# Kernel tuning notes

Hardware: AMD Instinct MI355X
Metric: run time of the kernel (lower is better)

Reference implementation:

```python
import jax, jax.numpy as jnp
import numpy as np

N_NODES = 50000
N_GRAPHS = 64
IN_DIM, HIDDEN, OUT_DIM = 2063, 256, 128
E_L, E_G = 800000, 1600000


def setup_inputs() -> dict:
    key = jax.random.key(0)
    ks = jax.random.split(key, 16)
    x = jax.random.normal(ks[0], (N_NODES, IN_DIM), dtype=jnp.float32)
    edge_index_l = jax.random.randint(ks[1], (2, E_L), 0, N_NODES, dtype=jnp.int64)
    edge_index_g = jax.random.randint(ks[2], (2, E_G), 0, N_NODES, dtype=jnp.int64)
    batch = jnp.sort(jax.random.randint(ks[3], (N_NODES,), 0, N_GRAPHS, dtype=jnp.int64))

    def glorot(k, shape):
        scale = jnp.sqrt(2.0 / (shape[0] + shape[1])).astype(jnp.float32)
        return jax.random.normal(k, shape, dtype=jnp.float32) * scale

    return {
        "x": x,
        "edge_index_l": edge_index_l,
        "edge_index_g": edge_index_g,
        "batch": batch,
        "W_l1": glorot(ks[4], (IN_DIM, HIDDEN)), "b_l1": jnp.zeros((HIDDEN,), jnp.float32),
        "W_l2": glorot(ks[5], (HIDDEN, OUT_DIM)), "b_l2": jnp.zeros((OUT_DIM,), jnp.float32),
        "W_g1": glorot(ks[6], (IN_DIM, HIDDEN)), "b_g1": jnp.zeros((HIDDEN,), jnp.float32),
        "W_g2": glorot(ks[7], (HIDDEN, OUT_DIM)), "b_g2": jnp.zeros((OUT_DIM,), jnp.float32),
        "W_fuse": glorot(ks[8], (2 * OUT_DIM, OUT_DIM)), "b_fuse": jnp.zeros((OUT_DIM,), jnp.float32),
    }


def gcn_conv(x, edge_index, W, b):
    # PyG GCNConv: add self loops, symmetric D^{-1/2}(A+I)D^{-1/2} normalization,
    # linear transform then scatter-add aggregation at target nodes.
    n = x.shape[0]
    loops = jnp.arange(n, dtype=edge_index.dtype)
    src = jnp.concatenate([edge_index[0], loops])
    dst = jnp.concatenate([edge_index[1], loops])
    deg = jax.ops.segment_sum(jnp.ones_like(dst, dtype=x.dtype), dst, num_segments=n)
    dinv = jax.lax.rsqrt(deg)  # deg >= 1 due to self loops
    norm = dinv[src] * dinv[dst]  # [E+n]
    h = x @ W  # [n, out]
    msg = h[src] * norm[:, None]  # gather + scale
    return jax.ops.segment_sum(msg, dst, num_segments=n) + b


def global_mean_pool(x, batch, num_graphs):
    sums = jax.ops.segment_sum(x, batch, num_segments=num_graphs)
    cnt = jax.ops.segment_sum(jnp.ones((x.shape[0],), x.dtype), batch, num_segments=num_graphs)
    return sums / jnp.maximum(cnt, 1.0)[:, None]


def reference(x, edge_index_l, edge_index_g, batch,
              W_l1, b_l1, W_l2, b_l2, W_g1, b_g1, W_g2, b_g2, W_fuse, b_fuse):
    # dropout is identity in eval mode
    xl = jax.nn.relu(gcn_conv(x, edge_index_l, W_l1, b_l1))
    xl = gcn_conv(xl, edge_index_l, W_l2, b_l2)
    xl = global_mean_pool(xl, batch, N_GRAPHS)

    xg = jax.nn.relu(gcn_conv(x, edge_index_g, W_g1, b_g1))
    xg = gcn_conv(xg, edge_index_g, W_g2, b_g2)
    xg = global_mean_pool(xg, batch, N_GRAPHS)

    out = jnp.concatenate([xl, xg], axis=1)  # [G, 2*out_dim]
    return jax.nn.relu(out @ W_fuse + b_fuse)
```

## Files before the change

kernel.cpp:

```cpp
#include <hip/hip_runtime.h>
#include <hip/hip_bf16.h>
#include <cstdint>
#include <cstddef>


#define N_NODES 50000
#define N_GRAPHS 64
#define IN_DIM 2063
#define HIDDEN 256
#define OUT_DIM 128
#define EDGES_L 800000
#define EDGES_G 1600000
#define HCOLS 512
#define KPAD 2112
#define MPAD 50048
#define PCH 256
#define NCHUNK ((N_NODES + PCH - 1) / PCH)

#define QUARTER 12544
#define SL_L 64
#define SL_G 128
#define EPS 12500
#define HBLOCKS (4 * (SL_L + SL_G))

typedef __attribute__((ext_vector_type(8))) __bf16 bf16x8;
typedef __attribute__((ext_vector_type(4))) float f32x4;

__device__ __forceinline__ float bf2f(unsigned short u) {
  union { unsigned int i; float f; } c; c.i = ((unsigned int)u) << 16; return c.f;
}
__device__ __forceinline__ unsigned short f2bf(float f) {
  __hip_bfloat16 h = __float2bfloat16(f);
  return *reinterpret_cast<unsigned short*>(&h);
}

__global__ void k_cvt_x(const float* __restrict__ x, unsigned short* __restrict__ xb) {
  const int G = KPAD / 4;
  long long i = (long long)blockIdx.x * blockDim.x + threadIdx.x;
  if (i >= (long long)MPAD * G) return;
  int row = (int)(i / G);
  int k = (int)(i - (long long)row * G) * 4;
  ushort4 o;
  float v0 = 0.f, v1 = 0.f, v2 = 0.f, v3 = 0.f;
  if (row < N_NODES) {
    const float* xr = x + (size_t)row * IN_DIM;
    if (k + 0 < IN_DIM) v0 = xr[k + 0];
    if (k + 1 < IN_DIM) v1 = xr[k + 1];
    if (k + 2 < IN_DIM) v2 = xr[k + 2];
    if (k + 3 < IN_DIM) v3 = xr[k + 3];
  }
  o.x = f2bf(v0); o.y = f2bf(v1); o.z = f2bf(v2); o.w = f2bf(v3);
  *(ushort4*)(xb + (size_t)row * KPAD + k) = o;
}

__global__ void k_cvt_w(const float* __restrict__ Wl, const float* __restrict__ Wg,
                        unsigned short* __restrict__ Wt) {
  int i = blockIdx.x * blockDim.x + threadIdx.x;
  if (i >= HCOLS * KPAD) return;
  int n = i / KPAD;
  int k = i - n * KPAD;
  float v = 0.f;
  if (k < IN_DIM) {
    v = (n < HIDDEN) ? Wl[(size_t)k * HIDDEN + n] : Wg[(size_t)k * HIDDEN + (n - HIDDEN)];
  }
  Wt[(size_t)n * KPAD + k] = f2bf(v);
}

__launch_bounds__(256)
__global__ void k_hist(const int* __restrict__ dstL, const int* __restrict__ dstG,
                       int* __restrict__ partL, int* __restrict__ partG) {
  __shared__ int hist[QUARTER];
  const int i = blockIdx.x;
  const int* __restrict__ dst;
  int slice, q;
  int* __restrict__ part;
  if (i < 4 * SL_L) {
    slice = i >> 2; q = i & 3;
    dst = dstL;
    part = partL + (size_t)(slice * 4 + q) * QUARTER;
  } else {
    int j = i - 4 * SL_L;
    slice = j >> 2; q = j & 3;
    dst = dstG;
    part = partG + (size_t)(slice * 4 + q) * QUARTER;
  }
  for (int t = threadIdx.x; t < QUARTER; t += 256) hist[t] = 0;
  __syncthreads();
  const int e0 = slice * EPS;
  const int qbase = q * QUARTER;
  for (int e = e0 + threadIdx.x; e < e0 + EPS; e += 256) {
    int d = dst[e] - qbase;
    if ((unsigned)d < QUARTER) atomicAdd(&hist[d], 1);
  }
  __syncthreads();
  for (int t = threadIdx.x; t < QUARTER; t += 256) part[t] = hist[t];
}

__global__ void k_prefix(int* __restrict__ partL, int* __restrict__ partG,
                         const int* __restrict__ batch, int* __restrict__ degL,
                         int* __restrict__ degG, float* __restrict__ dinvL,
                         float* __restrict__ dinvG, float* __restrict__ cL,
                         float* __restrict__ cG) {
  int t = blockIdx.x * blockDim.x + threadIdx.x;
  if (t >= 8 * QUARTER) return;
  const int b = t / (4 * QUARTER);
  const int n = t - b * 4 * QUARTER;
  const int q = n / QUARTER, loc = n - q * QUARTER;
  const int NS = b ? SL_G : SL_L;
  int* p = (b ? partG : partL) + (size_t)q * QUARTER + loc;
  int run = 0;
  for (int s = 0; s < NS; s++) {
    int* pp = p + (size_t)s * 4 * QUARTER;
    int v = *pp;
    *pp = run;
    run += v;
  }
  if (n < N_NODES) {
    float d = 1.0f / sqrtf((float)(run + 1));
    if (b == 0) {
      degL[n] = run; dinvL[n] = d; cL[(size_t)n * 64 + batch[n]] = d * d;
    } else {
      degG[n] = run; dinvG[n] = d; cG[(size_t)n * 64 + batch[n]] = d * d;
    }
  }
}

__global__ void k_bounds(const int* __restrict__ batch, int* __restrict__ start) {
  int n = blockIdx.x * blockDim.x + threadIdx.x;
  if (n >= N_NODES) return;
  int bn = batch[n];
  int bp = n ? batch[n - 1] : -1;
  for (int g = bp + 1; g <= bn; g++) start[g] = n;
  if (n == N_NODES - 1)
    for (int g = bn + 1; g <= N_GRAPHS; g++) start[g] = N_NODES;
}

__global__ void k_scan1(const int* __restrict__ degL, const int* __restrict__ degG,
                        int* __restrict__ rowL, int* __restrict__ rowG) {
  __shared__ int part[1024];
  const int t = threadIdx.x;
  const int* __restrict__ deg = blockIdx.x ? degG : degL;
  int* __restrict__ row = blockIdx.x ? rowG : rowL;
  const int c0 = t * 49;
  int s = 0;
  for (int j = 0; j < 49; j++) {
    int idx = c0 + j;
    s += (idx < N_NODES) ? deg[idx] : 0;
  }
  part[t] = s;
  __syncthreads();
  for (int ofs = 1; ofs < 1024; ofs <<= 1) {
    int v = (t >= ofs) ? part[t - ofs] : 0;
    __syncthreads();
    part[t] += v;
    __syncthreads();
  }
  int run = (t > 0) ? part[t - 1] : 0;
  for (int j = 0; j < 49; j++) {
    int idx = c0 + j;
    if (idx < N_NODES) { row[idx] = run; run += deg[idx]; }
  }
  if (t == 1023) row[N_NODES] = part[1023];
}

__launch_bounds__(256)
__global__ void k_scatter2(const int* __restrict__ srcL, const int* __restrict__ dstL,
                           const int* __restrict__ srcG, const int* __restrict__ dstG,
                           const int* __restrict__ partL, const int* __restrict__ partG,
                           const int* __restrict__ rowL, const int* __restrict__ rowG,
                           const float* __restrict__ dinvL, const float* __restrict__ dinvG,
                           const int* __restrict__ batch, int2* __restrict__ erL,
                           int2* __restrict__ erG, float* __restrict__ cL,
                           float* __restrict__ cG) {
  __shared__ int hist[QUARTER];
  const int i = blockIdx.x;
  const int *src, *dst, *part, *row;
  const float* dinv;
  int2* er;
  float* c;
  int slice, q;
  if (i < 4 * SL_L) {
    slice = i >> 2; q = i & 3;
    src = srcL; dst = dstL; row = rowL; dinv = dinvL; er = erL; c = cL;
    part = partL + (size_t)(slice * 4 + q) * QUARTER;
  } else {
    int j = i - 4 * SL_L;
    slice = j >> 2; q = j & 3;
    src = srcG; dst = dstG; row = rowG; dinv = dinvG; er = erG; c = cG;
    part = partG + (size_t)(slice * 4 + q) * QUARTER;
  }
  for (int t = threadIdx.x; t < QUARTER; t += 256) hist[t] = 0;
  __syncthreads();
  const int e0 = slice * EPS;
  const int qbase = q * QUARTER;
  for (int e = e0 + threadIdx.x; e < e0 + EPS; e += 256) {
    int d = dst[e];
    int loc = d - qbase;
    if ((unsigned)loc < QUARTER) {
      int s = src[e];
      int rank = atomicAdd(&hist[loc], 1);
      int pos = row[d] + part[loc] + rank;
      float nrm = dinv[s] * dinv[d];
      er[pos] = make_int2(s, __float_as_int(nrm));
      atomicAdd(&c[(size_t)s * 64 + batch[d]], nrm);
    }
  }
}

__launch_bounds__(256)
__global__ void k_mfma_gemm(const unsigned short* __restrict__ Xb,
                            const unsigned short* __restrict__ Wt,
                            unsigned short* __restrict__ H) {
  __shared__ __align__(16) char lds[32768];
  const int tid = threadIdx.x;
  const int lane = tid & 63;
  const int wave = tid >> 6;
  const int wr = wave >> 1, wc = wave & 1;
  const int brow = blockIdx.y * 128;
  const int bcol = blockIdx.x * 128;

  f32x4 acc[4][4];
  const f32x4 zero = {0.f, 0.f, 0.f, 0.f};
#pragma unroll
  for (int m = 0; m < 4; m++)
#pragma unroll
    for (int n = 0; n < 4; n++) acc[m][n] = zero;

  int rowA[4], kcS[4], ldsOff[4];
#pragma unroll
  for (int i = 0; i < 4; i++) {
    int s = (i * 4 + wave) * 64 + lane;
    int row = s >> 3;
    int c = s & 7;
    rowA[i] = row;
    kcS[i] = (c ^ (row & 7)) * 8;
    ldsOff[i] = ((i * 4 + wave) * 64) * 16;
  }

  const int fr = lane & 15;
  const int fq = lane >> 4;
  const int arow0 = wr * 64 + fr;
  const int brow0 = wc * 64 + fr;
  const int sw = lane & 7;

  for (int t = 0; t < KPAD / 64; ++t) {
    const int k0 = t * 64;
#pragma unroll
    for (int i = 0; i < 4; i++) {
      const unsigned short* g = Xb + (size_t)(brow + rowA[i]) * KPAD + k0 + kcS[i];
      __builtin_amdgcn_global_load_lds(
          (const __attribute__((address_space(1))) void*)g,
          (__attribute__((address_space(3))) void*)(lds + ldsOff[i]), 16, 0, 0);
    }
#pragma unroll
    for (int i = 0; i < 4; i++) {
      const unsigned short* g = Wt + (size_t)(bcol + rowA[i]) * KPAD + k0 + kcS[i];
      __builtin_amdgcn_global_load_lds(
          (const __attribute__((address_space(1))) void*)g,
          (__attribute__((address_space(3))) void*)(lds + 16384 + ldsOff[i]), 16, 0, 0);
    }
    __syncthreads();

#pragma unroll
    for (int kk = 0; kk < 2; kk++) {
      const int cidx = ((kk * 4 + fq) ^ sw) * 16;
      bf16x8 av[4], bv[4];
#pragma unroll
      for (int m = 0; m < 4; m++)
        av[m] = *(const bf16x8*)(lds + (arow0 + m * 16) * 128 + cidx);
#pragma unroll
      for (int n = 0; n < 4; n++)
        bv[n] = *(const bf16x8*)(lds + 16384 + (brow0 + n * 16) * 128 + cidx);
#pragma unroll
      for (int m = 0; m < 4; m++)
#pragma unroll
        for (int n = 0; n < 4; n++)
          acc[m][n] = __builtin_amdgcn_mfma_f32_16x16x32_bf16(av[m], bv[n], acc[m][n], 0, 0, 0);
    }
    __syncthreads();
  }

#pragma unroll
  for (int m = 0; m < 4; m++) {
    const int r0 = brow + wr * 64 + m * 16 + fq * 4;
#pragma unroll
    for (int n = 0; n < 4; n++) {
      const int col = bcol + wc * 64 + n * 16 + fr;
#pragma unroll
      for (int j = 0; j < 4; j++) {
        int r = r0 + j;
        if (r < N_NODES) H[(size_t)r * HCOLS + col] = f2bf(acc[m][n][j]);
      }
    }
  }
}

__global__ void k_agg(const unsigned short* __restrict__ h,
                      const float* __restrict__ dinvL, const float* __restrict__ dinvG,
                      const int* __restrict__ rowL, const int* __restrict__ rowG,
                      const int2* __restrict__ erL, const int2* __restrict__ erG,
                      const float* __restrict__ biasL, const float* __restrict__ biasG,
                      unsigned short* __restrict__ xl) {
  const int br = blockIdx.y;
  const int node = blockIdx.x * 4 + (threadIdx.x >> 6);
  const int lane = threadIdx.x & 63;
  const float* __restrict__ dinv = br ? dinvG : dinvL;
  const int* __restrict__ rp = br ? rowG : rowL;
  const int2* __restrict__ er = br ? erG : erL;
  const float* __restrict__ bias = br ? biasG : biasL;
  const int off = br ? 256 : 0;
  const size_t lcol = off + lane * 4;

  float di = dinv[node];
  float w0 = di * di;
  ushort4 u = *(const ushort4*)(h + (size_t)node * HCOLS + lcol);
  float a0 = w0 * bf2f(u.x), a1 = w0 * bf2f(u.y), a2 = w0 * bf2f(u.z), a3 = w0 * bf2f(u.w);

  int e = rp[node];
  const int e1 = rp[node + 1];
  for (; e + 8 <= e1; e += 8) {
    int2 r[8];
    ushort4 v[8];
#pragma unroll
    for (int j = 0; j < 8; j++) r[j] = er[e + j];
#pragma unroll
    for (int j = 0; j < 8; j++)
      v[j] = *(const ushort4*)(h + (size_t)r[j].x * HCOLS + lcol);
#pragma unroll
    for (int j = 0; j < 8; j++) {
      float w = __int_as_float(r[j].y);
      a0 = fmaf(w, bf2f(v[j].x), a0);
      a1 = fmaf(w, bf2f(v[j].y), a1);
      a2 = fmaf(w, bf2f(v[j].z), a2);
      a3 = fmaf(w, bf2f(v[j].w), a3);
    }
  }
  for (; e + 4 <= e1; e += 4) {
    int2 r[4];
    ushort4 v[4];
#pragma unroll
    for (int j = 0; j < 4; j++) r[j] = er[e + j];
#pragma unroll
    for (int j = 0; j < 4; j++)
      v[j] = *(const ushort4*)(h + (size_t)r[j].x * HCOLS + lcol);
#pragma unroll
    for (int j = 0; j < 4; j++) {
      float w = __int_as_float(r[j].y);
      a0 = fmaf(w, bf2f(v[j].x), a0);
      a1 = fmaf(w, bf2f(v[j].y), a1);
      a2 = fmaf(w, bf2f(v[j].z), a2);
      a3 = fmaf(w, bf2f(v[j].w), a3);
    }
  }
  for (; e < e1; e++) {
    int2 r = er[e];
    float w = __int_as_float(r.y);
    ushort4 v = *(const ushort4*)(h + (size_t)r.x * HCOLS + lcol);
    a0 = fmaf(w, bf2f(v.x), a0);
    a1 = fmaf(w, bf2f(v.y), a1);
    a2 = fmaf(w, bf2f(v.z), a2);
    a3 = fmaf(w, bf2f(v.w), a3);
  }
  float4 b = *(const float4*)(bias + lane * 4);
  ushort4 o;
  o.x = f2bf(fmaxf(a0 + b.x, 0.f));
  o.y = f2bf(fmaxf(a1 + b.y, 0.f));
  o.z = f2bf(fmaxf(a2 + b.z, 0.f));
  o.w = f2bf(fmaxf(a3 + b.w, 0.f));
  *(ushort4*)(xl + (size_t)node * HCOLS + lcol) = o;
}

__launch_bounds__(256)
__global__ void k_pool2(const unsigned short* __restrict__ xl,
                        const float* __restrict__ cL, const float* __restrict__ cG,
                        float* __restrict__ Spart) {
  __shared__ float cs[64][64];
  const int t = threadIdx.x;
  const int chunk = blockIdx.x;
  const int br = blockIdx.y;
  const float* __restrict__ C = br ? cG : cL;
  const int xoff = br ? 256 : 0;
  const int n0 = chunk * PCH;
  float acc[64];
#pragma unroll
  for (int g = 0; g < 64; g++) acc[g] = 0.f;

  for (int tile = 0; tile < PCH; tile += 64) {
    const int base = n0 + tile;
    __syncthreads();
#pragma unroll
    for (int i = 0; i < 16; i++) {
      int idx = i * 256 + t;
      int nn = idx >> 6, gg = idx & 63;
      int node = base + nn;
      cs[nn][gg] = (node < N_NODES) ? C[(size_t)node * 64 + gg] : 0.f;
    }
    __syncthreads();
    for (int nn = 0; nn < 64; nn++) {
      int node = base + nn;
      float v = (node < N_NODES) ? bf2f(xl[(size_t)node * HCOLS + xoff + t]) : 0.f;
#pragma unroll
      for (int g4 = 0; g4 < 16; g4++) {
        float4 cv = *(const float4*)&cs[nn][g4 * 4];
        acc[g4 * 4 + 0] = fmaf(cv.x, v, acc[g4 * 4 + 0]);
        acc[g4 * 4 + 1] = fmaf(cv.y, v, acc[g4 * 4 + 1]);
        acc[g4 * 4 + 2] = fmaf(cv.z, v, acc[g4 * 4 + 2]);
        acc[g4 * 4 + 3] = fmaf(cv.w, v, acc[g4 * 4 + 3]);
      }
    }
  }
  float* sp = Spart + ((size_t)br * NCHUNK + chunk) * 16384 + t;
#pragma unroll
  for (int g = 0; g < 64; g++) sp[g * 256] = acc[g];
}

__global__ void k_pool_reduce(const float* __restrict__ Spart, float* __restrict__ S) {
  int i = blockIdx.x * blockDim.x + threadIdx.x;
  if (i >= 2 * 16384) return;
  int br = i >> 14, idx = i & 16383;
  const float* p = Spart + (size_t)br * NCHUNK * 16384 + idx;
  float s = 0.f;
  for (int ch = 0; ch < NCHUNK; ch++) s += p[(size_t)ch * 16384];
  S[i] = s;
}

__global__ void k_final(const float* __restrict__ S,
                        const float* __restrict__ Wl2, const float* __restrict__ bl2,
                        const float* __restrict__ Wg2, const float* __restrict__ bg2,
                        const float* __restrict__ Wf, const float* __restrict__ bf,
                        const int* __restrict__ start, float* __restrict__ out) {
  __shared__ float pl[OUT_DIM], pg[OUT_DIM];
  int g = blockIdx.x, t = threadIdx.x;
  float invc = 1.0f / fmaxf((float)(start[g + 1] - start[g]), 1.0f);
  const float* Sl = S + (size_t)g * HIDDEN;
  const float* Sg = S + (size_t)N_GRAPHS * HIDDEN + (size_t)g * HIDDEN;
  float al = 0.f, ag = 0.f;
  for (int k = 0; k < HIDDEN; k++) {
    al = fmaf(Sl[k], Wl2[k * OUT_DIM + t], al);
    ag = fmaf(Sg[k], Wg2[k * OUT_DIM + t], ag);
  }
  pl[t] = al * invc + bl2[t];
  pg[t] = ag * invc + bg2[t];
  __syncthreads();
  float o = bf[t];
  for (int j = 0; j < OUT_DIM; j++) {
    o = fmaf(pl[j], Wf[j * OUT_DIM + t], o);
    o = fmaf(pg[j], Wf[(OUT_DIM + j) * OUT_DIM + t], o);
  }
  out[(size_t)g * OUT_DIM + t] = fmaxf(o, 0.f);
}

extern "C" void kernel_launch(void* const* d_in, const int* in_sizes, int n_in,
                              void* d_out, int out_size, void* d_ws, size_t ws_size,
                              hipStream_t stream) {
  const float* x = (const float*)d_in[0];
  const int* el = (const int*)d_in[1];
  const int* eg = (const int*)d_in[2];
  const int* batch = (const int*)d_in[3];
  const float* Wl1 = (const float*)d_in[4];
  const float* bl1 = (const float*)d_in[5];
  const float* Wl2 = (const float*)d_in[6];
  const float* bl2 = (const float*)d_in[7];
  const float* Wg1 = (const float*)d_in[8];
  const float* bg1 = (const float*)d_in[9];
  const float* Wg2 = (const float*)d_in[10];
  const float* bg2 = (const float*)d_in[11];
  const float* Wf = (const float*)d_in[12];
  const float* bf = (const float*)d_in[13];
  float* out = (float*)d_out;
  char* ws = (char*)d_ws;

  const size_t NPAD = 200192;
  size_t off = 0;
  float* c_l = (float*)(ws + off); off += (size_t)N_NODES * 64 * 4;
  float* c_g = (float*)(ws + off); off += (size_t)N_NODES * 64 * 4;
  const size_t zero_bytes = off;
  int* start = (int*)(ws + off); off += 512;
  float* S = (float*)(ws + off); off += (size_t)2 * N_GRAPHS * HIDDEN * 4;
  int* deg_l = (int*)(ws + off); off += NPAD;
  int* deg_g = (int*)(ws + off); off += NPAD;
  float* dinv_l = (float*)(ws + off); off += NPAD;
  float* dinv_g = (float*)(ws + off); off += NPAD;
  int* row_l = (int*)(ws + off); off += NPAD;
  int* row_g = (int*)(ws + off); off += NPAD;
  int* partL = (int*)(ws + off); off += (size_t)SL_L * 4 * QUARTER * 4;
  int* partG = (int*)(ws + off); off += (size_t)SL_G * 4 * QUARTER * 4;
  int2* er_l = (int2*)(ws + off); off += (size_t)EDGES_L * 8;
  int2* er_g = (int2*)(ws + off); off += (size_t)EDGES_G * 8;
  unsigned short* xb = (unsigned short*)(ws + off); off += (size_t)MPAD * KPAD * 2;
  unsigned short* Wt = (unsigned short*)(ws + off); off += (size_t)HCOLS * KPAD * 2;
  unsigned short* h = (unsigned short*)(ws + off); off += (size_t)N_NODES * HCOLS * 2;
  unsigned short* xl = (unsigned short*)(ws + off); off += (size_t)N_NODES * HCOLS * 2;
  float* Spart = (float*)xb;

  const int* srcL = el;
  const int* dstL = el + EDGES_L;
  const int* srcG = eg;
  const int* dstG = eg + EDGES_G;

  hipMemsetAsync(ws, 0, zero_bytes, stream);

  {
    long long tot = (long long)MPAD * (KPAD / 4);
    k_cvt_x<<<(int)((tot + 255) / 256), 256, 0, stream>>>(x, xb);
    k_cvt_w<<<(HCOLS * KPAD + 255) / 256, 256, 0, stream>>>(Wl1, Wg1, Wt);
  }

  k_hist<<<HBLOCKS, 256, 0, stream>>>(dstL, dstG, partL, partG);
  k_prefix<<<(8 * QUARTER + 255) / 256, 256, 0, stream>>>(partL, partG, batch, deg_l, deg_g,
                                                          dinv_l, dinv_g, c_l, c_g);
  k_bounds<<<(N_NODES + 255) / 256, 256, 0, stream>>>(batch, start);
  k_scan1<<<2, 1024, 0, stream>>>(deg_l, deg_g, row_l, row_g);
  k_scatter2<<<HBLOCKS, 256, 0, stream>>>(srcL, dstL, srcG, dstG, partL, partG, row_l, row_g,
                                          dinv_l, dinv_g, batch, er_l, er_g, c_l, c_g);

  dim3 ggrid(4, MPAD / 128);
  k_mfma_gemm<<<ggrid, 256, 0, stream>>>(xb, Wt, h);

  dim3 agrid(N_NODES / 4, 2);
  k_agg<<<agrid, 256, 0, stream>>>(h, dinv_l, dinv_g, row_l, row_g, er_l, er_g, bl1, bg1, xl);

  dim3 pgrid(NCHUNK, 2);
  k_pool2<<<pgrid, 256, 0, stream>>>(xl, c_l, c_g, Spart);
  k_pool_reduce<<<(2 * 16384 + 255) / 256, 256, 0, stream>>>(Spart, S);

  k_final<<<N_GRAPHS, OUT_DIM, 0, stream>>>(S, Wl2, bl2, Wg2, bg2, Wf, bf, start, out);
}
```

Measured before the change: 1.036 ms.

## Fuse fp32-to-bf16 conversion of x into the GEMM and merge bounds kernel into scan

Removes the separate pass that converts x to a padded bf16 buffer. The GEMM now reads fp32 rows of x directly, converts them in registers and writes them to LDS, prefetching the next k-slice during compute. The GEMM tile becomes 64 rows by all 512 columns so each x row is read only once, with W streamed per block. The graph-bounds kernel is folded into the scan launch as extra blocks. The trade-offs are unaligned fp32 row loads, heavier W traffic per block and 72KB of LDS per block, which limits occupancy.

After: 958.8 us. 1.08x faster.

```diff
diff --git a/kernel.cpp b/kernel.cpp
--- a/kernel.cpp
+++ b/kernel.cpp
@@ -14,6 +14,7 @@
 #define HCOLS 512
 #define KPAD 2112
 #define MPAD 50048
+#define GBM 64
 #define PCH 256
 #define NCHUNK ((N_NODES + PCH - 1) / PCH)
 
@@ -32,25 +33,6 @@
 __device__ __forceinline__ unsigned short f2bf(float f) {
   __hip_bfloat16 h = __float2bfloat16(f);
   return *reinterpret_cast<unsigned short*>(&h);
-}
-
-__global__ void k_cvt_x(const float* __restrict__ x, unsigned short* __restrict__ xb) {
-  const int G = KPAD / 4;
-  long long i = (long long)blockIdx.x * blockDim.x + threadIdx.x;
-  if (i >= (long long)MPAD * G) return;
-  int row = (int)(i / G);
-  int k = (int)(i - (long long)row * G) * 4;
-  ushort4 o;
-  float v0 = 0.f, v1 = 0.f, v2 = 0.f, v3 = 0.f;
-  if (row < N_NODES) {
-    const float* xr = x + (size_t)row * IN_DIM;
-    if (k + 0 < IN_DIM) v0 = xr[k + 0];
-    if (k + 1 < IN_DIM) v1 = xr[k + 1];
-    if (k + 2 < IN_DIM) v2 = xr[k + 2];
-    if (k + 3 < IN_DIM) v3 = xr[k + 3];
-  }
-  o.x = f2bf(v0); o.y = f2bf(v1); o.z = f2bf(v2); o.w = f2bf(v3);
-  *(ushort4*)(xb + (size_t)row * KPAD + k) = o;
 }
 
 __global__ void k_cvt_w(const float* __restrict__ Wl, const float* __restrict__ Wg,
@@ -125,18 +107,19 @@
   }
 }
 
-__global__ void k_bounds(const int* __restrict__ batch, int* __restrict__ start) {
-  int n = blockIdx.x * blockDim.x + threadIdx.x;
-  if (n >= N_NODES) return;
-  int bn = batch[n];
-  int bp = n ? batch[n - 1] : -1;
-  for (int g = bp + 1; g <= bn; g++) start[g] = n;
-  if (n == N_NODES - 1)
-    for (int g = bn + 1; g <= N_GRAPHS; g++) start[g] = N_NODES;
-}
-
 __global__ void k_scan1(const int* __restrict__ degL, const int* __restrict__ degG,
-                        int* __restrict__ rowL, int* __restrict__ rowG) {
+                        int* __restrict__ rowL, int* __restrict__ rowG,
+                        const int* __restrict__ batch, int* __restrict__ start) {
+  if (blockIdx.x >= 2) {
+    int n = (blockIdx.x - 2) * 1024 + threadIdx.x;
+    if (n >= N_NODES) return;
+    int bn = batch[n];
+    int bp = n ? batch[n - 1] : -1;
+    for (int g = bp + 1; g <= bn; g++) start[g] = n;
+    if (n == N_NODES - 1)
+      for (int g = bn + 1; g <= N_GRAPHS; g++) start[g] = N_NODES;
+    return;
+  }
   __shared__ int part[1024];
   const int t = threadIdx.x;
   const int* __restrict__ deg = blockIdx.x ? degG : degL;
@@ -207,85 +190,105 @@
   }
 }
 
-__launch_bounds__(256)
-__global__ void k_mfma_gemm(const unsigned short* __restrict__ Xb,
+__launch_bounds__(256, 2)
+__global__ void k_mfma_gemm(const float* __restrict__ X,
                             const unsigned short* __restrict__ Wt,
                             unsigned short* __restrict__ H) {
-  __shared__ __align__(16) char lds[32768];
+  __shared__ __align__(16) char lds[8192 + 65536];
   const int tid = threadIdx.x;
   const int lane = tid & 63;
   const int wave = tid >> 6;
-  const int wr = wave >> 1, wc = wave & 1;
-  const int brow = blockIdx.y * 128;
-  const int bcol = blockIdx.x * 128;
-
-  f32x4 acc[4][4];
-  const f32x4 zero = {0.f, 0.f, 0.f, 0.f};
-#pragma unroll
-  for (int m = 0; m < 4; m++)
-#pragma unroll
-    for (int n = 0; n < 4; n++) acc[m][n] = zero;
-
-  int rowA[4], kcS[4], ldsOff[4];
-#pragma unroll
-  for (int i = 0; i < 4; i++) {
-    int s = (i * 4 + wave) * 64 + lane;
-    int row = s >> 3;
-    int c = s & 7;
-    rowA[i] = row;
-    kcS[i] = (c ^ (row & 7)) * 8;
-    ldsOff[i] = ((i * 4 + wave) * 64) * 16;
-  }
+  const int brow = blockIdx.x * GBM;
+
+  const int ar = tid >> 2;
+  const int ak = (tid & 3) * 16;
+  const int arow_g = brow + ar;
+  const bool aok = arow_g < N_NODES;
+  const float* __restrict__ Arow = X + (size_t)arow_g * IN_DIM;
+  const int ac0 = (tid & 3) * 2;
+  char* const awr0 = lds + ar * 128 + ((ac0 ^ (ar & 7)) * 16);
+  char* const awr1 = lds + ar * 128 + (((ac0 + 1) ^ (ar & 7)) * 16);
 
   const int fr = lane & 15;
   const int fq = lane >> 4;
-  const int arow0 = wr * 64 + fr;
-  const int brow0 = wc * 64 + fr;
-  const int sw = lane & 7;
+
+  f32x4 acc[4][8];
+  const f32x4 zero = {0.f, 0.f, 0.f, 0.f};
+#pragma unroll
+  for (int m = 0; m < 4; m++)
+#pragma unroll
+    for (int n = 0; n < 8; n++) acc[m][n] = zero;
+
+  float a[16];
+#pragma unroll
+  for (int j = 0; j < 16; j++) a[j] = aok ? Arow[ak + j] : 0.f;
 
   for (int t = 0; t < KPAD / 64; ++t) {
     const int k0 = t * 64;
 #pragma unroll
-    for (int i = 0; i < 4; i++) {
-      const unsigned short* g = Xb + (size_t)(brow + rowA[i]) * KPAD + k0 + kcS[i];
+    for (int i = 0; i < 16; i++) {
+      const int s = i * 256 + wave * 64 + lane;
+      const int row = s >> 3, cch = s & 7;
+      const unsigned short* g = Wt + (size_t)row * KPAD + k0 + ((cch ^ (row & 7)) * 8);
       __builtin_amdgcn_global_load_lds(
           (const __attribute__((address_space(1))) void*)g,
-          (__attribute__((address_space(3))) void*)(lds + ldsOff[i]), 16, 0, 0);
-    }
-#pragma unroll
-    for (int i = 0; i < 4; i++) {
-      const unsigned short* g = Wt + (size_t)(bcol + rowA[i]) * KPAD + k0 + kcS[i];
-      __builtin_amdgcn_global_load_lds(
-          (const __attribute__((address_space(1))) void*)g,
-          (__attribute__((address_space(3))) void*)(lds + 16384 + ldsOff[i]), 16, 0, 0);
+          (__attribute__((address_space(3))) void*)(lds + 8192 + (i * 256 + wave * 64) * 16),
+          16, 0, 0);
+    }
+    {
+      uint u0 = (uint)f2bf(a[0]) | ((uint)f2bf(a[1]) << 16);
+      uint u1 = (uint)f2bf(a[2]) | ((uint)f2bf(a[3]) << 16);
+      uint u2 = (uint)f2bf(a[4]) | ((uint)f2bf(a[5]) << 16);
+      uint u3 = (uint)f2bf(a[6]) | ((uint)f2bf(a[7]) << 16);
+      uint u4 = (uint)f2bf(a[8]) | ((uint)f2bf(a[9]) << 16);
+      uint u5 = (uint)f2bf(a[10]) | ((uint)f2bf(a[11]) << 16);
+      uint u6 = (uint)f2bf(a[12]) | ((uint)f2bf(a[13]) << 16);
+      uint u7 = (uint)f2bf(a[14]) | ((uint)f2bf(a[15]) << 16);
+      *(uint4*)awr0 = make_uint4(u0, u1, u2, u3);
+      *(uint4*)awr1 = make_uint4(u4, u5, u6, u7);
     }
     __syncthreads();
 
+    if (t + 1 < KPAD / 64) {
+      const int kb = k0 + 64 + ak;
+      if (aok) {
+        if (kb + 15 < IN_DIM) {
+#pragma unroll
+          for (int j = 0; j < 16; j++) a[j] = Arow[kb + j];
+        } else {
+#pragma unroll
+          for (int j = 0; j < 16; j++) a[j] = (kb + j < IN_DIM) ? Arow[kb + j] : 0.f;
+        }
+      }
+    }
+
 #pragma unroll
     for (int kk = 0; kk < 2; kk++) {
-      const int cidx = ((kk * 4 + fq) ^ sw) * 16;
-      bf16x8 av[4], bv[4];
-#pragma unroll
-      for (int m = 0; m < 4; m++)
-        av[m] = *(const bf16x8*)(lds + (arow0 + m * 16) * 128 + cidx);
-#pragma unroll
-      for (int n = 0; n < 4; n++)
-        bv[n] = *(const bf16x8*)(lds + 16384 + (brow0 + n * 16) * 128 + cidx);
-#pragma unroll
-      for (int m = 0; m < 4; m++)
-#pragma unroll
-        for (int n = 0; n < 4; n++)
-          acc[m][n] = __builtin_amdgcn_mfma_f32_16x16x32_bf16(av[m], bv[n], acc[m][n], 0, 0, 0);
+      const int kc = kk * 4 + fq;
+      bf16x8 bv[8];
+#pragma unroll
+      for (int n = 0; n < 8; n++) {
+        const int row = wave * 128 + n * 16 + fr;
+        bv[n] = *(const bf16x8*)(lds + 8192 + row * 128 + ((kc ^ (row & 7)) * 16));
+      }
+#pragma unroll
+      for (int m = 0; m < 4; m++) {
+        const int row = m * 16 + fr;
+        bf16x8 av = *(const bf16x8*)(lds + row * 128 + ((kc ^ (row & 7)) * 16));
+#pragma unroll
+        for (int n = 0; n < 8; n++)
+          acc[m][n] = __builtin_amdgcn_mfma_f32_16x16x32_bf16(av, bv[n], acc[m][n], 0, 0, 0);
+      }
     }
     __syncthreads();
   }
 
 #pragma unroll
   for (int m = 0; m < 4; m++) {
-    const int r0 = brow + wr * 64 + m * 16 + fq * 4;
-#pragma unroll
-    for (int n = 0; n < 4; n++) {
-      const int col = bcol + wc * 64 + n * 16 + fr;
+    const int r0 = brow + m * 16 + fq * 4;
+#pragma unroll
+    for (int n = 0; n < 8; n++) {
+      const int col = wave * 128 + n * 16 + fr;
 #pragma unroll
       for (int j = 0; j < 4; j++) {
         int r = r0 + j;
@@ -487,11 +490,10 @@
   int* partG = (int*)(ws + off); off += (size_t)SL_G * 4 * QUARTER * 4;
   int2* er_l = (int2*)(ws + off); off += (size_t)EDGES_L * 8;
   int2* er_g = (int2*)(ws + off); off += (size_t)EDGES_G * 8;
-  unsigned short* xb = (unsigned short*)(ws + off); off += (size_t)MPAD * KPAD * 2;
   unsigned short* Wt = (unsigned short*)(ws + off); off += (size_t)HCOLS * KPAD * 2;
   unsigned short* h = (unsigned short*)(ws + off); off += (size_t)N_NODES * HCOLS * 2;
   unsigned short* xl = (unsigned short*)(ws + off); off += (size_t)N_NODES * HCOLS * 2;
-  float* Spart = (float*)xb;
+  float* Spart = (float*)partL;
 
   const int* srcL = el;
   const int* dstL = el + EDGES_L;
@@ -500,22 +502,16 @@
 
   hipMemsetAsync(ws, 0, zero_bytes, stream);
 
-  {
-    long long tot = (long long)MPAD * (KPAD / 4);
-    k_cvt_x<<<(int)((tot + 255) / 256), 256, 0, stream>>>(x, xb);
-    k_cvt_w<<<(HCOLS * KPAD + 255) / 256, 256, 0, stream>>>(Wl1, Wg1, Wt);
-  }
+  k_cvt_w<<<(HCOLS * KPAD + 255) / 256, 256, 0, stream>>>(Wl1, Wg1, Wt);
 
   k_hist<<<HBLOCKS, 256, 0, stream>>>(dstL, dstG, partL, partG);
   k_prefix<<<(8 * QUARTER + 255) / 256, 256, 0, stream>>>(partL, partG, batch, deg_l, deg_g,
                                                           dinv_l, dinv_g, c_l, c_g);
-  k_bounds<<<(N_NODES + 255) / 256, 256, 0, stream>>>(batch, start);
-  k_scan1<<<2, 1024, 0, stream>>>(deg_l, deg_g, row_l, row_g);
+  k_scan1<<<51, 1024, 0, stream>>>(deg_l, deg_g, row_l, row_g, batch, start);
   k_scatter2<<<HBLOCKS, 256, 0, stream>>>(srcL, dstL, srcG, dstG, partL, partG, row_l, row_g,
                                           dinv_l, dinv_g, batch, er_l, er_g, c_l, c_g);
 
-  dim3 ggrid(4, MPAD / 128);
-  k_mfma_gemm<<<ggrid, 256, 0, stream>>>(xb, Wt, h);
+  k_mfma_gemm<<<MPAD / GBM, 256, 0, stream>>>(x, Wt, h);
 
   dim3 agrid(N_NODES / 4, 2);
   k_agg<<<agrid, 256, 0, stream>>>(h, dinv_l, dinv_g, row_l, row_g, er_l, er_g, bl1, bg1, xl);
```
